# Optimization experiments

Hardware: AMD Instinct MI355X
Metric: run time of the kernel (lower is better)

The kernel has to match this reference:

```python
import jax, jax.numpy as jnp
import numpy as np

CUTOFF = 5.0  # Angstrom, matches init kwarg
N_ATOMS = 1024
BOX = 30.0  # approx cubic box edge length


def setup_inputs() -> dict:
    key = jax.random.key(0)
    k1, k2 = jax.random.split(key)
    # fractional coordinates in [0,1)
    frac = jax.random.uniform(k1, (N_ATOMS, 3), dtype=jnp.float32)
    # slightly perturbed (triclinic-ish) ~30 A cell
    cell = BOX * jnp.eye(3, dtype=jnp.float32) + 0.5 * jax.random.normal(k2, (3, 3), dtype=jnp.float32)
    return {"frac": frac, "cell": cell}


def reference(frac, cell):
    """Periodic radius graph: masked displacement vectors under PBC.

    Returns masked_disp [N, N, 27, 3]: displacement r_j + S@cell - r_i for every
    (i, j, image shift S) pair within the cutoff, zero elsewhere (edge mask applied).
    This is the dense, jit-compatible encoding of the variable-length edge list the
    torch module produces (edges = nonzero entries, edge vectors = the values).
    """
    # 27 integer image shifts in {-1,0,1}^3
    s = np.array([-1, 0, 1])
    shifts_np = np.stack(np.meshgrid(s, s, s, indexing="ij"), axis=-1).reshape(-1, 3)
    shifts = jnp.asarray(shifts_np, dtype=frac.dtype)          # [27, 3]
    zero_shift = jnp.asarray(np.all(shifts_np == 0, axis=-1))  # [27] bool

    cart = frac @ cell            # [N, 3] cartesian positions
    shift_cart = shifts @ cell    # [27, 3] image translation vectors

    # disp[i, j, s] = cart[j] + shift_cart[s] - cart[i]  -> [N, N, 27, 3]
    disp = cart[None, :, None, :] + shift_cart[None, None, :, :] - cart[:, None, None, :]
    dist2 = jnp.sum(disp * disp, axis=-1)  # [N, N, 27]

    n = frac.shape[0]
    # exclude self-edge only in the zero-shift image (atom to its own periodic images is allowed)
    self_mask = jnp.eye(n, dtype=bool)[:, :, None] & zero_shift[None, None, :]
    mask = (dist2 < jnp.asarray(CUTOFF * CUTOFF, dtype=dist2.dtype)) & (~self_mask)

    masked_disp = jnp.where(mask[..., None], disp, jnp.zeros((), dtype=disp.dtype))
    return masked_disp
```

## Files before the change

### kernel.cpp

```cpp
#include <hip/hip_runtime.h>


static constexpr int N    = 1024;
static constexpr int CPR  = 27 * N;
static constexpr int HALF = CPR / 2;
static constexpr int TPB  = 256;
static constexpr int ITERS = HALF / TPB;

__global__ __launch_bounds__(TPB, 8)
void prg_kernel(const float* __restrict__ frac,
                const float* __restrict__ cell,
                float* __restrict__ out) {
  __shared__ float4 cartL[N];
  __shared__ float4 shiftL[27];

  const int tid = threadIdx.x;
  const int i   = blockIdx.x >> 1;
  const int h   = blockIdx.x & 1;

  const float c00 = cell[0], c01 = cell[1], c02 = cell[2];
  const float c10 = cell[3], c11 = cell[4], c12 = cell[5];
  const float c20 = cell[6], c21 = cell[7], c22 = cell[8];

  for (int r = tid; r < N; r += TPB) {
    const float f0 = frac[3*r], f1 = frac[3*r+1], f2 = frac[3*r+2];
    float x = __fmul_rn(f0, c00); x = fmaf(f1, c10, x); x = fmaf(f2, c20, x);
    float y = __fmul_rn(f0, c01); y = fmaf(f1, c11, y); y = fmaf(f2, c21, y);
    float z = __fmul_rn(f0, c02); z = fmaf(f1, c12, z); z = fmaf(f2, c22, z);
    cartL[r] = make_float4(x, y, z, 0.0f);
  }
  if (tid < 27) {
    const float sx = (float)(tid / 9 - 1);
    const float sy = (float)((tid / 3) % 3 - 1);
    const float sz = (float)(tid % 3 - 1);
    float x = __fmul_rn(sx, c00); x = fmaf(sy, c10, x); x = fmaf(sz, c20, x);
    float y = __fmul_rn(sx, c01); y = fmaf(sy, c11, y); y = fmaf(sz, c21, y);
    float z = __fmul_rn(sx, c02); z = fmaf(sy, c12, z); z = fmaf(sz, c22, z);
    shiftL[tid] = make_float4(x, y, z, 0.0f);
  }
  __syncthreads();

  const float4 ci = cartL[i];

  const int base = h * HALF + tid;
  float* orow = out + (size_t)i * (size_t)(CPR * 3);

  #pragma unroll 2
  for (int k = 0; k < ITERS; ++k) {
    const unsigned local = (unsigned)(base + k * TPB);
    const unsigned j = local / 27u;
    const unsigned s = local - j * 27u;

    const float4 cj = cartL[j];
    const float4 sh = shiftL[s];

    const float d0 = __fsub_rn(__fadd_rn(cj.x, sh.x), ci.x);
    const float d1 = __fsub_rn(__fadd_rn(cj.y, sh.y), ci.y);
    const float d2 = __fsub_rn(__fadd_rn(cj.z, sh.z), ci.z);

    const float dist2 = __fadd_rn(
        __fadd_rn(__fmul_rn(d0, d0), __fmul_rn(d1, d1)), __fmul_rn(d2, d2));

    const bool ok = (dist2 < 25.0f) && !((j == (unsigned)i) && (s == 13u));

    float* p = orow + 3u * local;
    p[0] = ok ? d0 : 0.0f;
    p[1] = ok ? d1 : 0.0f;
    p[2] = ok ? d2 : 0.0f;
  }
}

extern "C" void kernel_launch(void* const* d_in, const int* in_sizes, int n_in,
                              void* d_out, int out_size, void* d_ws, size_t ws_size,
                              hipStream_t stream) {
  const float* frac = (const float*)d_in[0];
  const float* cell = (const float*)d_in[1];
  float* out = (float*)d_out;
  prg_kernel<<<2 * N, TPB, 0, stream>>>(frac, cell, out);
}
```

Baseline: 358.9 us.

## Split into prep kernel and flat float4-store main kernel over output

A one-block prep kernel now writes the cartesian positions and shift vectors to workspace, so each block no longer rebuilds them in shared memory. The main kernel assigns each thread four consecutive output floats and writes them with one float4 store instead of three scalar stores. Each thread keeps its (j, s) pair fixed and steps i by 32 rows across 32 iterations. This targets store efficiency and the redundant per-block setup, at the cost of a second launch, global/L2 reads for the i positions, and select logic to pack two spanning cells into each float4.

Measured after the change: 338.2 us. -5.8%, faster.

```diff
diff --git a/kernel.cpp b/kernel.cpp
--- a/kernel.cpp
+++ b/kernel.cpp
@@ -1,72 +1,97 @@
 #include <hip/hip_runtime.h>
 
 
-static constexpr int N    = 1024;
-static constexpr int CPR  = 27 * N;
-static constexpr int HALF = CPR / 2;
-static constexpr int TPB  = 256;
-static constexpr int ITERS = HALF / TPB;
+static constexpr int N      = 1024;
+static constexpr int TPB    = 256;
+static constexpr int BLOCKS = 2592;
+static constexpr int ITERS  = 32;
+static constexpr unsigned NT      = (unsigned)BLOCKS * TPB;
+static constexpr unsigned DSTRIDE = 4u * NT;
+static constexpr unsigned ISTRIDE = 32u;
 
-__global__ __launch_bounds__(TPB, 8)
-void prg_kernel(const float* __restrict__ frac,
-                const float* __restrict__ cell,
-                float* __restrict__ out) {
-  __shared__ float4 cartL[N];
-  __shared__ float4 shiftL[27];
-
-  const int tid = threadIdx.x;
-  const int i   = blockIdx.x >> 1;
-  const int h   = blockIdx.x & 1;
-
+__global__ __launch_bounds__(1024)
+void prg_prep(const float* __restrict__ frac, const float* __restrict__ cell,
+              float4* __restrict__ ws) {
+  const int t = threadIdx.x;
   const float c00 = cell[0], c01 = cell[1], c02 = cell[2];
   const float c10 = cell[3], c11 = cell[4], c12 = cell[5];
   const float c20 = cell[6], c21 = cell[7], c22 = cell[8];
+  {
+    const float f0 = frac[3*t], f1 = frac[3*t+1], f2 = frac[3*t+2];
+    float x = __fmul_rn(f0,c00); x = fmaf(f1,c10,x); x = fmaf(f2,c20,x);
+    float y = __fmul_rn(f0,c01); y = fmaf(f1,c11,y); y = fmaf(f2,c21,y);
+    float z = __fmul_rn(f0,c02); z = fmaf(f1,c12,z); z = fmaf(f2,c22,z);
+    ws[t] = make_float4(x,y,z,0.f);
+  }
+  if (t < 27) {
+    const float sx = (float)(t/9 - 1), sy = (float)((t/3)%3 - 1), sz = (float)(t%3 - 1);
+    float x = __fmul_rn(sx,c00); x = fmaf(sy,c10,x); x = fmaf(sz,c20,x);
+    float y = __fmul_rn(sx,c01); y = fmaf(sy,c11,y); y = fmaf(sz,c21,y);
+    float z = __fmul_rn(sx,c02); z = fmaf(sy,c12,z); z = fmaf(sz,c22,z);
+    ws[N + t] = make_float4(x,y,z,0.f);
+  }
+}
 
-  for (int r = tid; r < N; r += TPB) {
-    const float f0 = frac[3*r], f1 = frac[3*r+1], f2 = frac[3*r+2];
-    float x = __fmul_rn(f0, c00); x = fmaf(f1, c10, x); x = fmaf(f2, c20, x);
-    float y = __fmul_rn(f0, c01); y = fmaf(f1, c11, y); y = fmaf(f2, c21, y);
-    float z = __fmul_rn(f0, c02); z = fmaf(f1, c12, z); z = fmaf(f2, c22, z);
-    cartL[r] = make_float4(x, y, z, 0.0f);
-  }
-  if (tid < 27) {
-    const float sx = (float)(tid / 9 - 1);
-    const float sy = (float)((tid / 3) % 3 - 1);
-    const float sz = (float)(tid % 3 - 1);
-    float x = __fmul_rn(sx, c00); x = fmaf(sy, c10, x); x = fmaf(sz, c20, x);
-    float y = __fmul_rn(sx, c01); y = fmaf(sy, c11, y); y = fmaf(sz, c21, y);
-    float z = __fmul_rn(sx, c02); z = fmaf(sy, c12, z); z = fmaf(sz, c22, z);
-    shiftL[tid] = make_float4(x, y, z, 0.0f);
-  }
-  __syncthreads();
+__global__ __launch_bounds__(TPB)
+void prg_main(const float4* __restrict__ ws, float* __restrict__ out) {
+  const unsigned T  = blockIdx.x * TPB + threadIdx.x;
+  const unsigned D0 = 4u * T;
+  const unsigned cellA = D0 / 3u;
+  const unsigned r     = D0 - 3u*cellA;
+  const unsigned c27A  = cellA / 27u;
+  const unsigned sA    = cellA - 27u*c27A;
+  const unsigned jA    = c27A & 1023u;
+  unsigned       iA    = c27A >> 10;
+  const bool wrapA     = (sA == 26u);
+  const unsigned c27B  = c27A + (wrapA ? 1u : 0u);
+  const unsigned sB    = wrapA ? 0u : (sA + 1u);
+  const unsigned jB    = c27B & 1023u;
+  unsigned       iB    = c27B >> 10;
 
-  const float4 ci = cartL[i];
+  const float4 cjA = ws[jA],     cjB = ws[jB];
+  const float4 shA = ws[N + sA], shB = ws[N + sB];
+  const float pAx = __fadd_rn(cjA.x, shA.x);
+  const float pAy = __fadd_rn(cjA.y, shA.y);
+  const float pAz = __fadd_rn(cjA.z, shA.z);
+  const float pBx = __fadd_rn(cjB.x, shB.x);
+  const float pBy = __fadd_rn(cjB.y, shB.y);
+  const float pBz = __fadd_rn(cjB.z, shB.z);
+  const unsigned jSelfA = (sA == 13u) ? jA : 0xFFFFFFFFu;
+  const unsigned jSelfB = (sB == 13u) ? jB : 0xFFFFFFFFu;
+  const bool r0 = (r == 0u), r1 = (r == 1u);
 
-  const int base = h * HALF + tid;
-  float* orow = out + (size_t)i * (size_t)(CPR * 3);
+  float* outp = out + (size_t)D0;
 
   #pragma unroll 2
   for (int k = 0; k < ITERS; ++k) {
-    const unsigned local = (unsigned)(base + k * TPB);
-    const unsigned j = local / 27u;
-    const unsigned s = local - j * 27u;
+    const float4 ciA = ws[iA];
+    const float4 ciB = ws[iB];
 
-    const float4 cj = cartL[j];
-    const float4 sh = shiftL[s];
+    float a0 = __fsub_rn(pAx, ciA.x);
+    float a1 = __fsub_rn(pAy, ciA.y);
+    float a2 = __fsub_rn(pAz, ciA.z);
+    const float da = __fadd_rn(
+        __fadd_rn(__fmul_rn(a0,a0), __fmul_rn(a1,a1)), __fmul_rn(a2,a2));
+    const bool oka = (da < 25.0f) && (jSelfA != iA);
+    a0 = oka ? a0 : 0.f; a1 = oka ? a1 : 0.f; a2 = oka ? a2 : 0.f;
 
-    const float d0 = __fsub_rn(__fadd_rn(cj.x, sh.x), ci.x);
-    const float d1 = __fsub_rn(__fadd_rn(cj.y, sh.y), ci.y);
-    const float d2 = __fsub_rn(__fadd_rn(cj.z, sh.z), ci.z);
+    float b0 = __fsub_rn(pBx, ciB.x);
+    float b1 = __fsub_rn(pBy, ciB.y);
+    float b2 = __fsub_rn(pBz, ciB.z);
+    const float db = __fadd_rn(
+        __fadd_rn(__fmul_rn(b0,b0), __fmul_rn(b1,b1)), __fmul_rn(b2,b2));
+    const bool okb = (db < 25.0f) && (jSelfB != iB);
+    b0 = okb ? b0 : 0.f; b1 = okb ? b1 : 0.f; b2 = okb ? b2 : 0.f;
 
-    const float dist2 = __fadd_rn(
-        __fadd_rn(__fmul_rn(d0, d0), __fmul_rn(d1, d1)), __fmul_rn(d2, d2));
+    float4 w;
+    w.x = r0 ? a0 : (r1 ? a1 : a2);
+    w.y = r0 ? a1 : (r1 ? a2 : b0);
+    w.z = r0 ? a2 : (r1 ? b0 : b1);
+    w.w = r0 ? b0 : (r1 ? b1 : b2);
 
-    const bool ok = (dist2 < 25.0f) && !((j == (unsigned)i) && (s == 13u));
-
-    float* p = orow + 3u * local;
-    p[0] = ok ? d0 : 0.0f;
-    p[1] = ok ? d1 : 0.0f;
-    p[2] = ok ? d2 : 0.0f;
+    *reinterpret_cast<float4*>(outp) = w;
+    outp += (size_t)DSTRIDE;
+    iA += ISTRIDE; iB += ISTRIDE;
   }
 }
 
@@ -75,6 +100,8 @@
                               hipStream_t stream) {
   const float* frac = (const float*)d_in[0];
   const float* cell = (const float*)d_in[1];
+  float4* ws = (float4*)d_ws;
   float* out = (float*)d_out;
-  prg_kernel<<<2 * N, TPB, 0, stream>>>(frac, cell, out);
+  prg_prep<<<1, 1024, 0, stream>>>(frac, cell, ws);
+  prg_main<<<BLOCKS, TPB, 0, stream>>>(ws, out);
 }
```
